# Kernel tuning notes

Measured on AMD Instinct MI355X. Metric: run time of the kernel, lower is better.

## Reference

```python
import jax, jax.numpy as jnp
import numpy as np

D_MODEL = 512; D_STATE = 128; D_CONV = 4; EXPAND = 2; HEADDIM = 64; CHUNK = 64
D_INNER = EXPAND * D_MODEL            # 1024
NHEADS = D_INNER // HEADDIM           # 16
CONV_DIM = D_INNER + 2 * D_STATE      # 1280
D_IN_PROJ = 2 * D_INNER + 2 * D_STATE + NHEADS  # 2320
BATCH, SEQLEN = 2, 8192


def setup_inputs() -> dict:
    key = jax.random.key(0)
    ks = jax.random.split(key, 8)
    s = 0.02
    return {
        "x": jax.random.normal(ks[0], (BATCH, SEQLEN, D_MODEL), jnp.float32),
        "in_proj_w": jax.random.normal(ks[1], (D_IN_PROJ, D_MODEL), jnp.float32) * s,
        "conv_w": jax.random.normal(ks[2], (CONV_DIM, 1, D_CONV), jnp.float32) * s,
        "conv_b": jnp.zeros((CONV_DIM,), jnp.float32),
        "dt_bias": jax.random.normal(ks[3], (NHEADS,), jnp.float32) * s,
        "A_log": jnp.log(jnp.arange(1, NHEADS + 1, dtype=jnp.float32)),
        "D_skip": jnp.ones((NHEADS,), jnp.float32),
        "norm_w": jnp.ones((D_INNER,), jnp.float32),
        "ssm_out_w": jax.random.normal(ks[4], (D_MODEL, D_INNER), jnp.float32) * s,
        "fuse_w": jax.random.normal(ks[5], (D_MODEL, 2 * D_MODEL), jnp.float32) * s,
        "fuse_b": jnp.zeros((D_MODEL,), jnp.float32),
    }


def segsum(a):
    # a: (..., T) -> (..., T, T) with [i, j] = sum_{j < d <= i} a[d]; -inf above diag
    T = a.shape[-1]
    a = jnp.broadcast_to(a[..., :, None], a.shape + (T,))
    a = jnp.where(jnp.tril(jnp.ones((T, T), bool), -1), a, 0.0)
    a = jnp.cumsum(a, axis=-2)
    return jnp.where(jnp.tril(jnp.ones((T, T), bool), 0), a, -jnp.inf)


def ssd(x, A, B, C):
    # x: (b,l,h,p), A: (b,l,h), B/C: (b,l,n) (single group, broadcast over heads)
    b, l, h, p = x.shape
    c = l // CHUNK
    x = x.reshape(b, c, CHUNK, h, p)
    A = jnp.transpose(A.reshape(b, c, CHUNK, h), (0, 3, 1, 2))   # (b,h,c,s)
    B = B.reshape(b, c, CHUNK, -1)
    C = C.reshape(b, c, CHUNK, -1)
    A_cumsum = jnp.cumsum(A, axis=-1)                             # (b,h,c,s)
    L = jnp.exp(segsum(A))                                        # (b,h,c,s,s) intra-chunk decay
    Y_diag = jnp.einsum("bcln,bcsn,bhcls,bcshp->bclhp", C, B, L, x)
    decay_states = jnp.exp(A_cumsum[..., -1:] - A_cumsum)         # (b,h,c,s)
    states = jnp.einsum("bcln,bhcl,bclhp->bchpn", B, decay_states, x)
    init = jnp.zeros_like(states[:, :1])
    A_pad = jnp.pad(A_cumsum[..., -1], ((0, 0), (0, 0), (1, 0)))  # (b,h,c+1)
    decay_chunk = jnp.exp(segsum(A_pad))                          # (b,h,c+1,c+1)
    new_states = jnp.einsum("bhzc,bchpn->bzhpn", decay_chunk,
                            jnp.concatenate([init, states], axis=1))
    states = new_states[:, :-1]                                   # state entering each chunk
    state_decay_out = jnp.exp(A_cumsum)
    Y_off = jnp.einsum("bchpn,bcsn,bhcs->bcshp", states, C, state_decay_out)
    return (Y_diag + Y_off).reshape(b, l, h, p)


def mamba2_block(u, in_proj_w, conv_w, conv_b, dt_bias, A_log, D_skip, norm_w, ssm_out_w):
    b, l, _ = u.shape
    zxbcdt = u @ in_proj_w.T                                      # (b,l,2320)
    z = zxbcdt[..., :D_INNER]
    xBC = zxbcdt[..., D_INNER:D_INNER + CONV_DIM]
    dt = jax.nn.softplus(zxbcdt[..., -NHEADS:] + dt_bias)         # (b,l,h)
    # depthwise causal conv over time
    conv = jax.lax.conv_general_dilated(
        jnp.transpose(xBC, (0, 2, 1)), conv_w, (1,), [(D_CONV - 1, 0)],
        dimension_numbers=("NCH", "OIH", "NCH"), feature_group_count=CONV_DIM)
    xBC = jax.nn.silu(jnp.transpose(conv + conv_b[None, :, None], (0, 2, 1)))
    xh = xBC[..., :D_INNER].reshape(b, l, NHEADS, HEADDIM)
    Bm = xBC[..., D_INNER:D_INNER + D_STATE]
    Cm = xBC[..., -D_STATE:]
    A = -jnp.exp(A_log)                                           # (h,)
    y = ssd(xh * dt[..., None], A * dt, Bm, Cm)
    y = y + xh * D_skip[None, None, :, None]
    y = y.reshape(b, l, D_INNER)
    # gated RMSNorm
    y = y * jax.nn.silu(z)
    y = y * jax.lax.rsqrt(jnp.mean(y * y, axis=-1, keepdims=True) + 1e-5) * norm_w
    return y @ ssm_out_w.T


def reference(x, in_proj_w, conv_w, conv_b, dt_bias, A_log, D_skip, norm_w,
              ssm_out_w, fuse_w, fuse_b):
    args = (in_proj_w, conv_w, conv_b, dt_bias, A_log, D_skip, norm_w, ssm_out_w)
    y_fwd = mamba2_block(x, *args)
    y_rev = jnp.flip(mamba2_block(jnp.flip(x, 1), *args), 1)
    y_cat = jnp.concatenate([y_fwd, y_rev], axis=-1)
    return y_cat @ fuse_w.T + fuse_b
```

## Files before the change

kernel.cpp:

```cpp
#include <hip/hip_runtime.h>
#include <cstddef>

#define B_SZ     2
#define L_SEQ    8192
#define D_INNERC 1024
#define NHEADSC  16
#define CHUNKC   64
#define NCHUNKC  128
#define CONV_DIMC 1280
#define D_PROJC  2320
#define M_ROWS   16384

typedef unsigned short bfu;

using bf16x8 = __attribute__((ext_vector_type(8))) short;
using f32x4  = __attribute__((ext_vector_type(4))) float;

__device__ __forceinline__ float silu_(float v) { return v / (1.f + expf(-v)); }

__device__ __forceinline__ float b2f(bfu u) {
  return __uint_as_float((unsigned)u << 16);
}
__device__ __forceinline__ bfu f2b(float f) {
  unsigned x = __float_as_uint(f);
  return (bfu)((x + 0x7fffu + ((x >> 16) & 1u)) >> 16);
}

__device__ __forceinline__ float4 ld4(const float* p) { return *(const float4*)p; }
__device__ __forceinline__ float4 ld4(const bfu* p) {
  ushort4 u = *(const ushort4*)p;
  float4 f;
  f.x = b2f(u.x); f.y = b2f(u.y); f.z = b2f(u.z); f.w = b2f(u.w);
  return f;
}
__device__ __forceinline__ void st4(float* p, float4 v) { *(float4*)p = v; }
__device__ __forceinline__ void st4(bfu* p, float4 v) {
  ushort4 u;
  u.x = f2b(v.x); u.y = f2b(v.y); u.z = f2b(v.z); u.w = f2b(v.w);
  *(ushort4*)p = u;
}

__device__ __forceinline__ void gl_lds16(const bfu* g, bfu* l) {
  __builtin_amdgcn_global_load_lds(
      (const __attribute__((address_space(1))) unsigned int*)g,
      (__attribute__((address_space(3))) unsigned int*)l, 16, 0, 0);
}

__device__ __forceinline__ int pos_of(int b, int c, int l, int dir) {
  int t = c * CHUNKC + l;
  return dir ? (b * L_SEQ + (L_SEQ - 1) - t) : (b * L_SEQ + t);
}

__global__ __launch_bounds__(256)
void mfma_nt(const bfu* __restrict__ A, int lda,
             const bfu* __restrict__ Bw, int ldb,
             void* __restrict__ Cv, int ldc,
             int N, int K, const float* __restrict__ bias, int mode)
{
  __shared__ bfu As[128 * 32];
  __shared__ bfu Bs[128 * 32];
  const int tid  = threadIdx.x;
  const int lane = tid & 63;
  const int wave = __builtin_amdgcn_readfirstlane(tid >> 6);
  const int wm = wave & 1, wn = wave >> 1;

  const int num_n = gridDim.x;
  const int flat  = blockIdx.y * num_n + blockIdx.x;
  const int xcd   = flat & 7;
  const int g     = flat >> 3;
  const int n0 = (g % num_n) * 128;
  const int m0 = ((g / num_n) * 8 + xcd) * 128;

  f32x4 acc[4][4];
#pragma unroll
  for (int i = 0; i < 4; ++i)
#pragma unroll
    for (int j = 0; j < 4; ++j)
      acc[i][j] = (f32x4){0.f, 0.f, 0.f, 0.f};

  const int srow = lane >> 2;
  const int scgp = lane & 3;

  for (int k0 = 0; k0 < K; k0 += 32) {
    __syncthreads();
#pragma unroll
    for (int si = 0; si < 2; ++si) {
      int s = wave * 2 + si;
      int r = s * 16 + srow;
      int cg = scgp ^ ((r >> 1) & 3);
      gl_lds16(A  + (size_t)(m0 + r) * lda + k0 + cg * 8, As + s * 512);
      gl_lds16(Bw + (size_t)(n0 + r) * ldb + k0 + cg * 8, Bs + s * 512);
    }
    __syncthreads();

    bf16x8 af[4], bfr[4];
#pragma unroll
    for (int i = 0; i < 4; ++i) {
      int ra = wm * 64 + i * 16 + (lane & 15);
      int ca = (lane >> 4) ^ ((ra >> 1) & 3);
      af[i] = *(const bf16x8*)(As + ra * 32 + ca * 8);
      int rb = wn * 64 + i * 16 + (lane & 15);
      int cb = (lane >> 4) ^ ((rb >> 1) & 3);
      bfr[i] = *(const bf16x8*)(Bs + rb * 32 + cb * 8);
    }
#pragma unroll
    for (int i = 0; i < 4; ++i)
#pragma unroll
      for (int j = 0; j < 4; ++j)
        acc[i][j] = __builtin_amdgcn_mfma_f32_16x16x32_bf16(af[i], bfr[j], acc[i][j], 0, 0, 0);
  }

#pragma unroll
  for (int i = 0; i < 4; ++i) {
    int mbase = m0 + wm * 64 + i * 16 + (lane >> 4) * 4;
#pragma unroll
    for (int j = 0; j < 4; ++j) {
      int n = n0 + wn * 64 + j * 16 + (lane & 15);
      if (n < N) {
#pragma unroll
        for (int r = 0; r < 4; ++r) {
          float v = acc[i][j][r];
          size_t off = (size_t)(mbase + r) * ldc + n;
          if (mode == 0) {
            ((bfu*)Cv)[off] = f2b(v);
          } else {
            float* cp = (float*)Cv + off;
            if (mode == 2) v += *cp;
            else if (bias) v += bias[n];
            *cp = v;
          }
        }
      }
    }
  }
}

__global__ __launch_bounds__(256)
void cvt_x_k(const float* __restrict__ in, bfu* __restrict__ out)
{
  int q = blockIdx.x * 256 + threadIdx.x;
  st4(out + (size_t)q * 4, ld4(in + (size_t)q * 4));
}

__global__ __launch_bounds__(256)
void cvt_w_k(const float* __restrict__ in, bfu* __restrict__ out)
{
  int q = blockIdx.x * 256 + threadIdx.x;
  int row = q >> 7, c4 = (q & 127) << 2;
  float4 v = {0.f, 0.f, 0.f, 0.f};
  if (row < D_PROJC) v = ld4(in + (size_t)row * 512 + c4);
  st4(out + (size_t)row * 512 + c4, v);
}

__global__ __launch_bounds__(256)
void transpose_k(const float* __restrict__ in, bfu* __restrict__ out)
{
  int idx = blockIdx.x * 256 + threadIdx.x;
  int j = idx >> 9, k = idx & 511;
  out[idx] = f2b(in[k * 1024 + j]);
}

__global__ __launch_bounds__(256)
void cvt_fuse_k(const float* __restrict__ in, bfu* __restrict__ out)
{
  int q = blockIdx.x * 256 + threadIdx.x;
  int m = q >> 7, kg = (q & 127) << 2;
  float4 v = ld4(in + (size_t)(m & 511) * 1024 + (m >> 9) * 512 + kg);
  st4(out + (size_t)m * 512 + kg, v);
}

__global__ __launch_bounds__(256)
void conv_k(const bfu* __restrict__ zx, const float* __restrict__ conv_w,
            const float* __restrict__ conv_b, bfu* __restrict__ xBC, int dir)
{
  int ch = blockIdx.x * 256 + threadIdx.x;
  int m0 = blockIdx.y * 8;
  int b  = m0 >> 13, tb = m0 & (L_SEQ - 1);
  float w0 = conv_w[ch * 4 + 0], w1 = conv_w[ch * 4 + 1];
  float w2 = conv_w[ch * 4 + 2], w3 = conv_w[ch * 4 + 3];
  float cb = conv_b[ch];
  const bfu* src = zx + 1024 + ch;
  const int shift = dir ? 0 : 3;

  float v[11];
#pragma unroll
  for (int i = 0; i < 11; ++i) {
    int tt = tb + i - shift;
    v[i] = (tt >= 0 && tt < L_SEQ)
         ? b2f(src[(size_t)(b * L_SEQ + tt) * D_PROJC]) : 0.f;
  }
#pragma unroll
  for (int j = 0; j < 8; ++j) {
    float acc = cb;
    if (dir == 0) {
      acc += w0 * v[j] + w1 * v[j + 1] + w2 * v[j + 2] + w3 * v[j + 3];
    } else {
      acc += w0 * v[j + 3] + w1 * v[j + 2] + w2 * v[j + 1] + w3 * v[j];
    }
    xBC[(size_t)(m0 + j) * CONV_DIMC + ch] = f2b(silu_(acc));
  }
}

__global__ __launch_bounds__(256)
void states_mfma_k(const bfu* __restrict__ zx, const bfu* __restrict__ xBC,
                   const float* __restrict__ dt_bias, const float* __restrict__ A_log,
                   float* __restrict__ acum_g, float* __restrict__ dt_g,
                   bfu* __restrict__ states, int dir)
{
  __shared__ bfu BT[128 * 72];
  __shared__ bfu xsT[64 * 72];
  __shared__ float scaleS[8 * 64];

  int bid = blockIdx.x;
  int hb = bid >> 8;
  int c = bid & 127, b = (bid >> 7) & 1;
  int tid = threadIdx.x, lane = tid & 63;
  int w = tid >> 6, q = lane >> 4, t = lane & 15;

#pragma unroll
  for (int rr = 0; rr < 2; ++rr) {
    int i = w + rr * 4;
    int h = hb * 8 + i;
    int l = lane;
    int pos = pos_of(b, c, l, dir);
    float dtr = b2f(zx[(size_t)pos * D_PROJC + 2304 + h]) + dt_bias[h];
    float dt = (dtr > 20.f) ? dtr : log1pf(expf(dtr));
    float a = -expf(A_log[h]) * dt;
#pragma unroll
    for (int off = 1; off < 64; off <<= 1) {
      float v = __shfl_up(a, off);
      if (l >= off) a += v;
    }
    float alast = __shfl(a, 63);
    int gi = ((b * NCHUNKC + c) * NHEADSC + h) * 64 + l;
    acum_g[gi] = a; dt_g[gi] = dt;
    scaleS[i * 64 + l] = dt * expf(alast - a);
  }

#pragma unroll
  for (int r = 0; r < 8; ++r) {
    int qq = tid + r * 256;
    int l = qq & 63, ng = qq >> 6;
    ushort4 v = *(const ushort4*)(xBC + (size_t)pos_of(b, c, l, dir) * CONV_DIMC + 1024 + ng * 4);
    BT[(ng * 4 + 0) * 72 + l] = v.x; BT[(ng * 4 + 1) * 72 + l] = v.y;
    BT[(ng * 4 + 2) * 72 + l] = v.z; BT[(ng * 4 + 3) * 72 + l] = v.w;
  }
  __syncthreads();

  for (int i = 0; i < 8; ++i) {
    int h = hb * 8 + i;
#pragma unroll
    for (int r = 0; r < 4; ++r) {
      int qq = tid + r * 256;
      int l = qq & 63, pg = qq >> 6;
      float s = scaleS[i * 64 + l];
      ushort4 v = *(const ushort4*)(xBC + (size_t)pos_of(b, c, l, dir) * CONV_DIMC + h * 64 + pg * 4);
      xsT[(pg * 4 + 0) * 72 + l] = f2b(b2f(v.x) * s);
      xsT[(pg * 4 + 1) * 72 + l] = f2b(b2f(v.y) * s);
      xsT[(pg * 4 + 2) * 72 + l] = f2b(b2f(v.z) * s);
      xsT[(pg * 4 + 3) * 72 + l] = f2b(b2f(v.w) * s);
    }
    __syncthreads();

    bf16x8 axs[2];
#pragma unroll
    for (int ks = 0; ks < 2; ++ks)
      axs[ks] = *(const bf16x8*)(xsT + (w * 16 + t) * 72 + ks * 32 + q * 8);

    f32x4 acc[8];
#pragma unroll
    for (int j = 0; j < 8; ++j) acc[j] = (f32x4){0.f, 0.f, 0.f, 0.f};
#pragma unroll
    for (int ks = 0; ks < 2; ++ks)
#pragma unroll
      for (int j = 0; j < 8; ++j) {
        bf16x8 bB = *(const bf16x8*)(BT + (j * 16 + t) * 72 + ks * 32 + q * 8);
        acc[j] = __builtin_amdgcn_mfma_f32_16x16x32_bf16(axs[ks], bB, acc[j], 0, 0, 0);
      }

    size_t base = ((size_t)(b * NCHUNKC + c) * NHEADSC + h) * 8192;
#pragma unroll
    for (int j = 0; j < 8; ++j)
#pragma unroll
      for (int r = 0; r < 4; ++r) {
        int p = w * 16 + q * 4 + r, n = j * 16 + t;
        states[base + p * 128 + n] = f2b(acc[j][r]);
      }
    __syncthreads();
  }
}

__global__ __launch_bounds__(256)
void scan_k(bfu* __restrict__ states, const float* __restrict__ acum_g)
{
  int bid = blockIdx.x;
  int eb = bid & 15, h = (bid >> 4) & 15, b = bid >> 8;
  int e = eb * 512 + threadIdx.x * 2;
  bfu* p0 = states + ((size_t)(b * NCHUNKC) * NHEADSC + h) * 8192 + e;
  const float* ac = acum_g + ((b * NCHUNKC) * NHEADSC + h) * 64 + 63;
  const size_t cstride = (size_t)NHEADSC * 8192;
  const int astride = NHEADSC * 64;

  float pre0 = 0.f, pre1 = 0.f;
  uint raw = *(const uint*)p0;
  float dcur = expf(ac[0]);
  for (int c = 0; c < NCHUNKC; ++c) {
    uint raw_next = 0; float dnext = 0.f;
    if (c < NCHUNKC - 1) {
      raw_next = *(const uint*)(p0 + (c + 1) * cstride);
      dnext = expf(ac[(c + 1) * astride]);
    }
    float v0 = b2f((bfu)(raw & 0xffff));
    float v1 = b2f((bfu)(raw >> 16));
    uint packed = (uint)f2b(pre0) | ((uint)f2b(pre1) << 16);
    *(uint*)(p0 + c * cstride) = packed;
    pre0 = v0 + dcur * pre0;
    pre1 = v1 + dcur * pre1;
    raw = raw_next; dcur = dnext;
  }
}

__global__ __launch_bounds__(256)
void y_mfma_k(const bfu* __restrict__ xBC, const bfu* __restrict__ states,
              const float* __restrict__ acum_g, const float* __restrict__ dt_g,
              const float* __restrict__ D_skip, bfu* __restrict__ ybuf, int dir)
{
  __shared__ bfu smem[30976];
  bfu* Cs  = smem;
  bfu* Bsc = smem + 8704;
  bfu* Ps  = smem + 17408;
  bfu* xhT = smem + 26112;
  float* acumH = (float*)(smem + 30720);
  float* dtH   = acumH + 64;

  int bid = blockIdx.x;
  int hb = bid >> 8;
  int c = bid & 127, b = (bid >> 7) & 1;
  int tid = threadIdx.x, lane = tid & 63;
  int w = tid >> 6, q = lane >> 4, t = lane & 15;

#pragma unroll
  for (int r = 0; r < 8; ++r) {
    int qq = tid + r * 256;
    int row = qq >> 5, grp = qq & 31;
    const bfu* src = xBC + (size_t)pos_of(b, c, row, dir) * CONV_DIMC;
    *(ushort4*)(Cs  + row * 136 + grp * 4) = *(const ushort4*)(src + 1152 + grp * 4);
    *(ushort4*)(Bsc + row * 136 + grp * 4) = *(const ushort4*)(src + 1024 + grp * 4);
  }
  __syncthreads();

  bf16x8 af[4];
#pragma unroll
  for (int ks = 0; ks < 4; ++ks)
    af[ks] = *(const bf16x8*)(Cs + (w * 16 + t) * 136 + ks * 32 + q * 8);

  f32x4 sacc[4];
#pragma unroll
  for (int j = 0; j < 4; ++j) sacc[j] = (f32x4){0.f, 0.f, 0.f, 0.f};
#pragma unroll
  for (int ks = 0; ks < 4; ++ks)
#pragma unroll
    for (int j = 0; j < 4; ++j) {
      bf16x8 bf = *(const bf16x8*)(Bsc + (j * 16 + t) * 136 + ks * 32 + q * 8);
      sacc[j] = __builtin_amdgcn_mfma_f32_16x16x32_bf16(af[ks], bf, sacc[j], 0, 0, 0);
    }

  for (int i = 0; i < 8; ++i) {
    int h = hb * 8 + i;
    __syncthreads();
    size_t pbase = ((size_t)(b * NCHUNKC + c) * NHEADSC + h) * 8192;
#pragma unroll
    for (int r = 0; r < 8; ++r) {
      int qq = tid + r * 256;
      int row = qq >> 5, grp = qq & 31;
      *(ushort4*)(Ps + row * 136 + grp * 4) =
          *(const ushort4*)(states + pbase + row * 128 + grp * 4);
    }
#pragma unroll
    for (int r = 0; r < 4; ++r) {
      int qq = tid + r * 256;
      int l = qq & 63, pg = qq >> 6;
      ushort4 v = *(const ushort4*)(xBC + (size_t)pos_of(b, c, l, dir) * CONV_DIMC + h * 64 + pg * 4);
      xhT[(pg * 4 + 0) * 72 + l] = v.x; xhT[(pg * 4 + 1) * 72 + l] = v.y;
      xhT[(pg * 4 + 2) * 72 + l] = v.z; xhT[(pg * 4 + 3) * 72 + l] = v.w;
    }
    if (tid < 64) {
      int gi = ((b * NCHUNKC + c) * NHEADSC + h) * 64 + tid;
      acumH[tid] = acum_g[gi]; dtH[tid] = dt_g[gi];
    }
    __syncthreads();

    f32x4 yacc[4];
#pragma unroll
    for (int j = 0; j < 4; ++j) yacc[j] = (f32x4){0.f, 0.f, 0.f, 0.f};
#pragma unroll
    for (int ks = 0; ks < 4; ++ks)
#pragma unroll
      for (int j = 0; j < 4; ++j) {
        bf16x8 bP = *(const bf16x8*)(Ps + (j * 16 + t) * 136 + ks * 32 + q * 8);
        yacc[j] = __builtin_amdgcn_mfma_f32_16x16x32_bf16(af[ks], bP, yacc[j], 0, 0, 0);
      }

    float Dh = D_skip[h];
    bfu* sc = Bsc;
#pragma unroll
    for (int j = 0; j < 4; ++j)
#pragma unroll
      for (int r = 0; r < 4; ++r) {
        int l = w * 16 + q * 4 + r, s = j * 16 + t;
        float v = 0.f;
        if (s <= l) v = sacc[j][r] * expf(acumH[l] - acumH[s]) * dtH[s];
        if (s == l) v += Dh;
        sc[l * 72 + s] = f2b(v);
      }

    f32x4 acc2[4];
    float dec[4];
#pragma unroll
    for (int r = 0; r < 4; ++r) dec[r] = expf(acumH[w * 16 + q * 4 + r]);
#pragma unroll
    for (int j = 0; j < 4; ++j)
#pragma unroll
      for (int r = 0; r < 4; ++r) acc2[j][r] = yacc[j][r] * dec[r];

#pragma unroll
    for (int ks = 0; ks < 2; ++ks) {
      bf16x8 asc = *(const bf16x8*)(sc + (w * 16 + t) * 72 + ks * 32 + q * 8);
#pragma unroll
      for (int j = 0; j < 4; ++j) {
        bf16x8 bx = *(const bf16x8*)(xhT + (j * 16 + t) * 72 + ks * 32 + q * 8);
        acc2[j] = __builtin_amdgcn_mfma_f32_16x16x32_bf16(asc, bx, acc2[j], 0, 0, 0);
      }
    }

#pragma unroll
    for (int j = 0; j < 4; ++j)
#pragma unroll
      for (int r = 0; r < 4; ++r) {
        int l = w * 16 + q * 4 + r, p = j * 16 + t;
        ybuf[(size_t)pos_of(b, c, l, dir) * D_INNERC + h * 64 + p] = f2b(acc2[j][r]);
      }
  }
}

__global__ __launch_bounds__(256)
void norm_k(bfu* __restrict__ ybuf, const bfu* __restrict__ zx,
            const float* __restrict__ norm_w)
{
  int m = blockIdx.x, tid = threadIdx.x;
  float4 y = ld4(ybuf + (size_t)m * D_INNERC + tid * 4);
  float4 z = ld4(zx + (size_t)m * D_PROJC + tid * 4);
  float4 g;
  g.x = y.x * silu_(z.x); g.y = y.y * silu_(z.y);
  g.z = y.z * silu_(z.z); g.w = y.w * silu_(z.w);
  float ss = g.x * g.x + g.y * g.y + g.z * g.z + g.w * g.w;
#pragma unroll
  for (int off = 32; off >= 1; off >>= 1) ss += __shfl_xor(ss, off);
  __shared__ float red[4];
  int wid = tid >> 6;
  if ((tid & 63) == 0) red[wid] = ss;
  __syncthreads();
  float tot = red[0] + red[1] + red[2] + red[3];
  float scale = rsqrtf(tot * (1.f / 1024.f) + 1e-5f);
  float4 w = *(const float4*)(norm_w + tid * 4);
  g.x *= scale * w.x; g.y *= scale * w.y; g.z *= scale * w.z; g.w *= scale * w.w;
  st4(ybuf + (size_t)m * D_INNERC + tid * 4, g);
}

extern "C" void kernel_launch(void* const* d_in, const int* in_sizes, int n_in,
                              void* d_out, int out_size, void* d_ws, size_t ws_size,
                              hipStream_t stream)
{
  const float* x         = (const float*)d_in[0];
  const float* in_proj_w = (const float*)d_in[1];
  const float* conv_w    = (const float*)d_in[2];
  const float* conv_b    = (const float*)d_in[3];
  const float* dt_bias   = (const float*)d_in[4];
  const float* A_log     = (const float*)d_in[5];
  const float* D_skip    = (const float*)d_in[6];
  const float* norm_w    = (const float*)d_in[7];
  const float* ssm_out_w = (const float*)d_in[8];
  const float* fuse_w    = (const float*)d_in[9];
  const float* fuse_b    = (const float*)d_in[10];
  float* out = (float*)d_out;

  bfu* zx     = (bfu*)d_ws;
  bfu* xBC    = zx     + (size_t)M_ROWS * D_PROJC;
  bfu* states = xBC    + (size_t)M_ROWS * CONV_DIMC;
  bfu* ybuf   = states + (size_t)33554432;
  float* acum = (float*)(ybuf + (size_t)M_ROWS * D_INNERC);
  float* dtg  = acum + 262144;
  bfu* ssmTb  = (bfu*)(dtg + 262144);
  bfu* fuseA  = ssmTb + 524288;
  bfu* wcmb   = fuseA + 524288;
  bfu* xb = states;
  bfu* wb = states + 8388608;

  cvt_x_k<<<8192, 256, 0, stream>>>(x, xb);
  cvt_w_k<<<1216, 256, 0, stream>>>(in_proj_w, wb);
  transpose_k<<<2048, 256, 0, stream>>>(ssm_out_w, ssmTb);
  cvt_fuse_k<<<512, 256, 0, stream>>>(fuse_w, fuseA);

  mfma_nt<<<dim3(8, 8), 256, 0, stream>>>(
      fuseA, 512, ssmTb, 512, wcmb, 1024, 1024, 512, nullptr, 0);

  mfma_nt<<<dim3(19, 128), 256, 0, stream>>>(
      xb, 512, wb, 512, zx, D_PROJC, D_PROJC, 512, nullptr, 0);

  for (int dir = 0; dir < 2; ++dir) {
    conv_k<<<dim3(5, 2048), 256, 0, stream>>>(zx, conv_w, conv_b, xBC, dir);
    states_mfma_k<<<512, 256, 0, stream>>>(zx, xBC, dt_bias, A_log, acum, dtg, states, dir);
    scan_k<<<512, 256, 0, stream>>>(states, acum);
    y_mfma_k<<<512, 256, 0, stream>>>(xBC, states, acum, dtg, D_skip, ybuf, dir);
    norm_k<<<M_ROWS, 256, 0, stream>>>(ybuf, zx, norm_w);
    mfma_nt<<<dim3(4, 128), 256, 0, stream>>>(
        ybuf, 1024, wcmb + (size_t)dir * 524288, 1024, out, 512,
        512, 1024, dir == 0 ? fuse_b : nullptr, dir == 0 ? 1 : 2);
  }
}
```

Measured before the change: 571.8 us.

## Widen GEMM K-step to 64 and stage epilogue through LDS for vector stores

The MFMA GEMM now loads 64-wide K tiles per iteration, using an 8-way XOR swizzle, which halves the number of barrier pairs per K loop. The epilogue writes accumulators into shared memory first and then issues coalesced 16-byte global stores, done in two halves for fp32 outputs. This is meant to cut synchronization overhead and the scattered 2- and 4-byte global writes. In exchange it uses 32 KB of LDS per block, which may lower occupancy, and adds barriers to the epilogue.

```diff
diff --git a/kernel.cpp b/kernel.cpp
--- a/kernel.cpp
+++ b/kernel.cpp
@@ -57,8 +57,9 @@
              void* __restrict__ Cv, int ldc,
              int N, int K, const float* __restrict__ bias, int mode)
 {
-  __shared__ bfu As[128 * 32];
-  __shared__ bfu Bs[128 * 32];
+  __shared__ bfu sh[16384];
+  bfu* As = sh;
+  bfu* Bs = sh + 8192;
   const int tid  = threadIdx.x;
   const int lane = tid & 63;
   const int wave = __builtin_amdgcn_readfirstlane(tid >> 6);
@@ -78,59 +79,99 @@
     for (int j = 0; j < 4; ++j)
       acc[i][j] = (f32x4){0.f, 0.f, 0.f, 0.f};
 
-  const int srow = lane >> 2;
-  const int scgp = lane & 3;
-
-  for (int k0 = 0; k0 < K; k0 += 32) {
-    __syncthreads();
-#pragma unroll
-    for (int si = 0; si < 2; ++si) {
-      int s = wave * 2 + si;
-      int r = s * 16 + srow;
-      int cg = scgp ^ ((r >> 1) & 3);
-      gl_lds16(A  + (size_t)(m0 + r) * lda + k0 + cg * 8, As + s * 512);
-      gl_lds16(Bw + (size_t)(n0 + r) * ldb + k0 + cg * 8, Bs + s * 512);
-    }
-    __syncthreads();
-
-    bf16x8 af[4], bfr[4];
-#pragma unroll
-    for (int i = 0; i < 4; ++i) {
-      int ra = wm * 64 + i * 16 + (lane & 15);
-      int ca = (lane >> 4) ^ ((ra >> 1) & 3);
-      af[i] = *(const bf16x8*)(As + ra * 32 + ca * 8);
-      int rb = wn * 64 + i * 16 + (lane & 15);
-      int cb = (lane >> 4) ^ ((rb >> 1) & 3);
-      bfr[i] = *(const bf16x8*)(Bs + rb * 32 + cb * 8);
-    }
+  const int ro   = lane >> 3;
+  const int slot = lane & 7;
+
+  for (int k0 = 0; k0 < K; k0 += 64) {
+    __syncthreads();
+#pragma unroll
+    for (int si = 0; si < 4; ++si) {
+      int r = wave * 32 + si * 8 + ro;
+      int cg = slot ^ (r & 7);
+      gl_lds16(A  + (size_t)(m0 + r) * lda + k0 + cg * 8, As + (wave * 32 + si * 8) * 64);
+      gl_lds16(Bw + (size_t)(n0 + r) * ldb + k0 + cg * 8, Bs + (wave * 32 + si * 8) * 64);
+    }
+    __syncthreads();
+
+#pragma unroll
+    for (int ks = 0; ks < 2; ++ks) {
+      bf16x8 af[4], bfr[4];
+#pragma unroll
+      for (int i = 0; i < 4; ++i) {
+        int ra = wm * 64 + i * 16 + (lane & 15);
+        int ca = (ks * 4 + (lane >> 4)) ^ (ra & 7);
+        af[i] = *(const bf16x8*)(As + ra * 64 + ca * 8);
+        int rb = wn * 64 + i * 16 + (lane & 15);
+        int cb = (ks * 4 + (lane >> 4)) ^ (rb & 7);
+        bfr[i] = *(const bf16x8*)(Bs + rb * 64 + cb * 8);
+      }
+#pragma unroll
+      for (int i = 0; i < 4; ++i)
+#pragma unroll
+        for (int j = 0; j < 4; ++j)
+          acc[i][j] = __builtin_amdgcn_mfma_f32_16x16x32_bf16(af[i], bfr[j], acc[i][j], 0, 0, 0);
+    }
+  }
+
+  __syncthreads();
+  if (mode == 0) {
 #pragma unroll
     for (int i = 0; i < 4; ++i)
 #pragma unroll
       for (int j = 0; j < 4; ++j)
-        acc[i][j] = __builtin_amdgcn_mfma_f32_16x16x32_bf16(af[i], bfr[j], acc[i][j], 0, 0, 0);
-  }
-
-#pragma unroll
-  for (int i = 0; i < 4; ++i) {
-    int mbase = m0 + wm * 64 + i * 16 + (lane >> 4) * 4;
-#pragma unroll
-    for (int j = 0; j < 4; ++j) {
-      int n = n0 + wn * 64 + j * 16 + (lane & 15);
-      if (n < N) {
 #pragma unroll
         for (int r = 0; r < 4; ++r) {
-          float v = acc[i][j][r];
-          size_t off = (size_t)(mbase + r) * ldc + n;
-          if (mode == 0) {
-            ((bfu*)Cv)[off] = f2b(v);
-          } else {
-            float* cp = (float*)Cv + off;
-            if (mode == 2) v += *cp;
-            else if (bias) v += bias[n];
-            *cp = v;
+          int ml = wm * 64 + i * 16 + (lane >> 4) * 4 + r;
+          int nl = wn * 64 + j * 16 + (lane & 15);
+          sh[ml * 128 + nl] = f2b(acc[i][j][r]);
+        }
+    __syncthreads();
+    bfu* Cb = (bfu*)Cv;
+#pragma unroll
+    for (int rr = 0; rr < 8; ++rr) {
+      int idx = rr * 256 + tid;
+      int row = idx >> 4, co = (idx & 15) * 8;
+      if (n0 + co < N) {
+        *(ulonglong2*)(Cb + (size_t)(m0 + row) * ldc + n0 + co) =
+            *(const ulonglong2*)(sh + row * 128 + co);
+      }
+    }
+  } else {
+    float* Cf = (float*)Cv;
+    float* shf = (float*)sh;
+#pragma unroll
+    for (int p = 0; p < 2; ++p) {
+      if (wm == p) {
+#pragma unroll
+        for (int i = 0; i < 4; ++i)
+#pragma unroll
+          for (int j = 0; j < 4; ++j)
+#pragma unroll
+            for (int r = 0; r < 4; ++r) {
+              int ml = i * 16 + (lane >> 4) * 4 + r;
+              int nl = wn * 64 + j * 16 + (lane & 15);
+              shf[ml * 128 + nl] = acc[i][j][r];
+            }
+      }
+      __syncthreads();
+#pragma unroll
+      for (int rr = 0; rr < 8; ++rr) {
+        int idx = rr * 256 + tid;
+        int row = idx >> 5, co = (idx & 31) * 4;
+        int n = n0 + co;
+        if (n < N) {
+          float4 v = *(float4*)(shf + row * 128 + co);
+          float* cp = Cf + (size_t)(m0 + p * 64 + row) * ldc + n;
+          if (mode == 2) {
+            float4 o = *(float4*)cp;
+            v.x += o.x; v.y += o.y; v.z += o.z; v.w += o.w;
+          } else if (bias) {
+            v.x += bias[n]; v.y += bias[n + 1]; v.z += bias[n + 2]; v.w += bias[n + 3];
           }
+          *(float4*)cp = v;
         }
       }
+      __syncthreads();
     }
   }
 }
```

Result: faster. 529.1 us (-7.5%).
